# Optimization experiments

Measured on AMD Instinct MI355X. Metric: run time of the kernel, lower is better.

Reference implementation:

```python
import jax, jax.numpy as jnp
import numpy as np

B, S, E = 2, 2048, 2048
HQ, HKV, D = 16, 4, 128
WINDOW = 512
ROPE_BASE = 10000.0


def apply_rope(x):
    # x: [B, H, S, D]; rotate-half RoPE, positions start at 0 (prefill, no cache)
    half = x.shape[-1] // 2
    inv_freq = 1.0 / (ROPE_BASE ** (jnp.arange(half, dtype=jnp.float32) / half))
    ang = jnp.arange(x.shape[2], dtype=jnp.float32)[:, None] * inv_freq[None, :]  # [S, half]
    cos, sin = jnp.cos(ang), jnp.sin(ang)
    x1, x2 = x[..., :half], x[..., half:]
    return jnp.concatenate([x1 * cos - x2 * sin, x1 * sin + x2 * cos], axis=-1)


def setup_inputs() -> dict:
    key = jax.random.key(0)
    ks = jax.random.split(key, 9)
    sc = 0.02
    return {
        "x": jax.random.normal(ks[0], (B, S, E), dtype=jnp.float32),
        "Wq": jax.random.normal(ks[1], (HQ * D, E), dtype=jnp.float32) * sc,
        "bq": jnp.zeros((HQ * D,), dtype=jnp.float32),
        "Wk": jax.random.normal(ks[2], (HKV * D, E), dtype=jnp.float32) * sc,
        "bk": jnp.zeros((HKV * D,), dtype=jnp.float32),
        "Wv": jax.random.normal(ks[3], (HKV * D, E), dtype=jnp.float32) * sc,
        "bv": jnp.zeros((HKV * D,), dtype=jnp.float32),
        "Wo": jax.random.normal(ks[4], (E, HQ * D), dtype=jnp.float32) * sc,
        "bo": jnp.zeros((E,), dtype=jnp.float32),
    }


def reference(x, Wq, bq, Wk, bk, Wv, bv, Wo, bo):
    b, s, _ = x.shape
    group = HQ // HKV
    # projections (torch Linear: y = x @ W.T + b)
    Q = (x @ Wq.T + bq).reshape(b, s, HQ, D).transpose(0, 2, 1, 3)     # [B,HQ,S,D]
    K = (x @ Wk.T + bk).reshape(b, s, HKV, D).transpose(0, 2, 1, 3)    # [B,HKV,S,D]
    V = (x @ Wv.T + bv).reshape(b, s, HKV, D).transpose(0, 2, 1, 3)
    Q = apply_rope(Q)
    K = apply_rope(K)
    # GQA: group query heads per KV head instead of repeating K/V (same math)
    Qg = Q.reshape(b, HKV, group, s, D)
    scores = jnp.einsum('bkgqd,bkyd->bkgqy', Qg, K) / jnp.sqrt(jnp.float32(D))
    # sliding-window causal mask: j <= i and i - j <= window_size
    i = jnp.arange(s)[:, None]
    j = jnp.arange(s)[None, :]
    allowed = (j <= i) & ((i - j) <= WINDOW)
    scores = jnp.where(allowed, scores, jnp.float32(-jnp.inf))
    w = jax.nn.softmax(scores, axis=-1)
    out = jnp.einsum('bkgqy,bkyd->bkgqd', w, V)                        # [B,HKV,G,S,D]
    out = out.reshape(b, HQ, s, D).transpose(0, 2, 1, 3).reshape(b, s, HQ * D)
    out = out @ Wo.T + bo  # dropout is identity at inference
    return out
```

## Files before the change

### kernel.cpp

```cpp
#include <hip/hip_runtime.h>
#include <hip/hip_bf16.h>

typedef unsigned short u16;
typedef unsigned int u32;
typedef __attribute__((ext_vector_type(4))) unsigned short ushort4_t;
typedef __attribute__((ext_vector_type(8))) short short8;
typedef __attribute__((ext_vector_type(4))) float f32x4;

#define B_ 2
#define S_ 2048
#define E_ 2048
#define HQ_ 16
#define HKV_ 4
#define D_ 128
#define WINDOW_ 512

static __device__ __forceinline__ float bf2f(u16 u) {
    union { unsigned int i; float f; } v; v.i = ((unsigned int)u) << 16; return v.f;
}
static __device__ __forceinline__ u16 f2bf(float f) {
    unsigned int x = __float_as_uint(f);
    unsigned int r = (x + 0x7fffu + ((x >> 16) & 1u)) >> 16;
    return (u16)r;
}

static __device__ __forceinline__ void gload_lds16(const u16* g, u16* l) {
    __builtin_amdgcn_global_load_lds(
        (const __attribute__((address_space(1))) unsigned int*)g,
        (__attribute__((address_space(3))) unsigned int*)l,
        16, 0, 0);
}

static __device__ __forceinline__ int detect_fp32(const u16* wq, int* cnt_sh) {
    if (threadIdx.x == 0) *cnt_sh = 0;
    __syncthreads();
    int c = 0;
    #pragma unroll
    for (int k = 0; k < 4; ++k) {
        u16 v = wq[threadIdx.x * 4 + k];
        if (((v >> 7) & 0xFF) >= 0x90) c++;
    }
    atomicAdd(cnt_sh, c);
    __syncthreads();
    return (*cnt_sh >= 64) ? 1 : 0;
}

#define C_WQ   8388608u
#define C_WK   12582912u
#define C_WV   13631488u
#define C_BQ   14680064u
#define C_BK   14682112u
#define C_BV   14682624u
#define C_WO   14683136u
#define C_BO   18877440u
#define NTOT   18879488u

__global__ __launch_bounds__(256) void convert_kernel(
    const void* p0, const void* p1, const void* p2, const void* p3, const void* p4,
    const void* p5, const void* p6, const void* p7, const void* p8,
    u16* __restrict__ C, int* __restrict__ flagout)
{
    __shared__ int cnt;
    const int f = detect_fp32((const u16*)p1, &cnt);
    if (blockIdx.x == 0 && threadIdx.x == 0) *flagout = f;

    unsigned int idx = (blockIdx.x * 256u + threadIdx.x) * 4u;
    if (idx >= NTOT) return;

    const void* src; unsigned int local;
    if      (idx < C_WQ) { src = p0; local = idx; }
    else if (idx < C_WK) { src = p1; local = idx - C_WQ; }
    else if (idx < C_WV) { src = p3; local = idx - C_WK; }
    else if (idx < C_BQ) { src = p5; local = idx - C_WV; }
    else if (idx < C_BK) { src = p2; local = idx - C_BQ; }
    else if (idx < C_BV) { src = p4; local = idx - C_BK; }
    else if (idx < C_WO) { src = p6; local = idx - C_BV; }
    else if (idx < C_BO) { src = p7; local = idx - C_WO; }
    else                 { src = p8; local = idx - C_BO; }

    ushort4_t o;
    if (f) {
        float4 v = *(const float4*)((const float*)src + local);
        o[0] = f2bf(v.x); o[1] = f2bf(v.y); o[2] = f2bf(v.z); o[3] = f2bf(v.w);
    } else {
        o = *(const ushort4_t*)((const u16*)src + local);
    }
    *(ushort4_t*)(C + idx) = o;
}

__global__ __launch_bounds__(512, 2) void gemm256(
    const u16* __restrict__ A, const u16* __restrict__ W,
    const u16* __restrict__ bias, u16* __restrict__ C,
    int M, int N, int K)
{
    __shared__ __align__(16) u16 lds[65536];

    const int m0 = blockIdx.y * 256, n0 = blockIdx.x * 256;
    const int t = threadIdx.x;
    const int wv = t >> 6, lane = t & 63;
    const int wm = wv >> 2, wn = wv & 3;
    const int quad = lane >> 4, l16 = lane & 15;
    const int h3 = l16 & 7;

    const int rr = t >> 3;
    const int sblk = ((t & 7) ^ (rr & 7)) * 8;

    const u16* Asrc = A + (size_t)(m0 + rr) * K + sblk;
    const u16* Bsrc = W + (size_t)(n0 + rr) * K + sblk;
    u16* ldsA = lds + wv * 512;
    u16* ldsB = lds + 16384 + wv * 512;

#define STAGE_A(slot, Qi, k0) gload_lds16(Asrc + (size_t)((Qi) * 64) * K + (k0), ldsA + (slot) * 32768 + (Qi) * 4096)
#define STAGE_B(slot, Qi, k0) gload_lds16(Bsrc + (size_t)((Qi) * 64) * K + (k0), ldsB + (slot) * 32768 + (Qi) * 4096)

    f32x4 acc[8][4];
    #pragma unroll
    for (int mi = 0; mi < 8; ++mi)
        #pragma unroll
        for (int ni = 0; ni < 4; ++ni)
            acc[mi][ni] = (f32x4){0.f, 0.f, 0.f, 0.f};

    const int NT = K / 64;

    #pragma unroll
    for (int q = 0; q < 4; ++q) STAGE_A(0, q, 0);
    #pragma unroll
    for (int q = 0; q < 4; ++q) STAGE_B(0, q, 0);
    __builtin_amdgcn_sched_barrier(0);
    STAGE_A(1, 0, 64);
    STAGE_A(1, 2, 64);
    __builtin_amdgcn_sched_barrier(0);

    short8 aA[4][2], aB[4][2];
    short8 b0[2][2], b1[2][2];

#define DSREAD_A(dst, qm_)                                                     \
    _Pragma("unroll")                                                          \
    for (int fr = 0; fr < 4; ++fr) {                                           \
        const int r = wm * 128 + (qm_) * 64 + fr * 16 + l16;                   \
        _Pragma("unroll")                                                      \
        for (int kk = 0; kk < 2; ++kk)                                         \
            dst[fr][kk] = *(const short8*)(As + r * 64 + (((kk * 4 + quad) ^ h3) << 3)); \
    }

#define DSREAD_B(dst, qn_)                                                     \
    _Pragma("unroll")                                                          \
    for (int g = 0; g < 2; ++g) {                                              \
        const int r = wn * 64 + (qn_) * 32 + g * 16 + l16;                     \
        _Pragma("unroll")                                                      \
        for (int kk = 0; kk < 2; ++kk)                                         \
            dst[g][kk] = *(const short8*)(Bs + r * 64 + (((kk * 4 + quad) ^ h3) << 3)); \
    }

#define MFMA_PH(qm_, afrag, bfrag, qn_)                                        \
    __builtin_amdgcn_s_setprio(1);                                             \
    _Pragma("unroll")                                                          \
    for (int g = 0; g < 2; ++g)                                                \
        _Pragma("unroll")                                                      \
        for (int fr = 0; fr < 4; ++fr)                                         \
            _Pragma("unroll")                                                  \
            for (int kk = 0; kk < 2; ++kk)                                     \
                acc[(qm_) * 4 + fr][(qn_) * 2 + g] =                           \
                    __builtin_amdgcn_mfma_f32_16x16x32_bf16(                   \
                        afrag[fr][kk], bfrag[g][kk], acc[(qm_) * 4 + fr][(qn_) * 2 + g], 0, 0, 0); \
    __builtin_amdgcn_s_setprio(0);

    for (int kt = 0; kt < NT; ++kt) {
        const int slot = kt & 1;
        const u16* As = lds + slot * 32768;
        const u16* Bs = As + 16384;

        if (kt == NT - 1) asm volatile("s_waitcnt vmcnt(0)" ::: "memory");
        else              asm volatile("s_waitcnt vmcnt(2)" ::: "memory");
        __builtin_amdgcn_s_barrier();
        __builtin_amdgcn_sched_barrier(0);

        const int kB = (kt + 1) * 64;
        const int kA = (kt + 2) * 64;
        const int sB = slot ^ 1;
        const bool doEarly = (kt <= NT - 2);
        const bool doMid   = (kt <= NT - 3);

        DSREAD_A(aA, 0);
        DSREAD_B(b0, 0);
        __builtin_amdgcn_sched_barrier(0);
        DSREAD_B(b1, 1);
        __builtin_amdgcn_sched_barrier(0);

        if (doEarly) { STAGE_A(sB, 1, kB); STAGE_A(sB, 3, kB);
                       STAGE_B(sB, 0, kB); STAGE_B(sB, 1, kB);
                       STAGE_B(sB, 2, kB); STAGE_B(sB, 3, kB); }
        __builtin_amdgcn_sched_barrier(0);

        asm volatile("s_waitcnt lgkmcnt(4)" ::: "memory");
        __builtin_amdgcn_sched_barrier(0);
        DSREAD_A(aB, 1);
        __builtin_amdgcn_sched_barrier(0);

        MFMA_PH(0, aA, b0, 0);
        __builtin_amdgcn_sched_barrier(0);
        asm volatile("s_waitcnt lgkmcnt(8)" ::: "memory");
        __builtin_amdgcn_sched_barrier(0);
        MFMA_PH(0, aA, b1, 1);
        __builtin_amdgcn_sched_barrier(0);
        asm volatile("s_waitcnt lgkmcnt(0)" ::: "memory");
        __builtin_amdgcn_sched_barrier(0);
        __builtin_amdgcn_s_barrier();
        __builtin_amdgcn_sched_barrier(0);

        if (doMid) { STAGE_A(slot, 0, kA); STAGE_A(slot, 2, kA); }
        __builtin_amdgcn_sched_barrier(0);

        MFMA_PH(1, aB, b1, 1);
        __builtin_amdgcn_sched_barrier(0);
        MFMA_PH(1, aB, b0, 0);
        __builtin_amdgcn_sched_barrier(0);
    }

#undef STAGE_A
#undef STAGE_B
#undef DSREAD_A
#undef DSREAD_B
#undef MFMA_PH

    #pragma unroll
    for (int mi = 0; mi < 8; ++mi) {
        #pragma unroll
        for (int ni = 0; ni < 4; ++ni) {
            const int row0 = m0 + wm * 128 + mi * 16 + quad * 4;
            const int col  = n0 + wn * 64 + ni * 16 + l16;
            const float bb = bf2f(bias[col]);
            #pragma unroll
            for (int r = 0; r < 4; ++r)
                C[(size_t)(row0 + r) * N + col] = f2bf(acc[mi][ni][r] + bb);
        }
    }
}

__global__ __launch_bounds__(512, 2) void gemm_out_p(
    const u16* __restrict__ A, const u16* __restrict__ W,
    const u16* __restrict__ bias, void* __restrict__ Cout,
    int M, int N, int K, const int* __restrict__ flagp)
{
    __shared__ __align__(16) u16 lds[49152];

    const int m0 = blockIdx.y * 128, n0 = blockIdx.x * 256;
    const int t = threadIdx.x;
    const int wv = t >> 6, lane = t & 63;
    const int wm = wv >> 2, wn = wv & 3;
    const int quad = lane >> 4, l16 = lane & 15;
    const int h3 = l16 & 7;

    const int rr = t >> 3;
    const int sblk = ((t & 7) ^ (rr & 7)) * 8;

    const u16* Asrc = A + (size_t)(m0 + rr) * K + sblk;
    const u16* Bsrc = W + (size_t)(n0 + rr) * K + sblk;
    u16* ldsA = lds + wv * 512;
    u16* ldsB = lds + 8192 + wv * 512;

#define STAGE_A(slot, Qi, k0) gload_lds16(Asrc + (size_t)((Qi) * 64) * K + (k0), ldsA + (slot) * 24576 + (Qi) * 4096)
#define STAGE_B(slot, Qi, k0) gload_lds16(Bsrc + (size_t)((Qi) * 64) * K + (k0), ldsB + (slot) * 24576 + (Qi) * 4096)

    f32x4 acc[4][4];
    #pragma unroll
    for (int mi = 0; mi < 4; ++mi)
        #pragma unroll
        for (int ni = 0; ni < 4; ++ni)
            acc[mi][ni] = (f32x4){0.f, 0.f, 0.f, 0.f};

    const int NT = K / 64;

    STAGE_A(0, 0, 0); STAGE_A(0, 1, 0);
    STAGE_B(0, 0, 0); STAGE_B(0, 1, 0); STAGE_B(0, 2, 0); STAGE_B(0, 3, 0);
    __builtin_amdgcn_sched_barrier(0);
    STAGE_A(1, 0, 64);
    __builtin_amdgcn_sched_barrier(0);

    short8 aA[4][2];
    short8 b0[2][2], b1[2][2];

#define DSREAD_A(dst)                                                          \
    _Pragma("unroll")                                                          \
    for (int fr = 0; fr < 4; ++fr) {                                           \
        const int r = wm * 64 + fr * 16 + l16;                                 \
        _Pragma("unroll")                                                      \
        for (int kk = 0; kk < 2; ++kk)                                         \
            dst[fr][kk] = *(const short8*)(As + r * 64 + (((kk * 4 + quad) ^ h3) << 3)); \
    }

#define DSREAD_B(dst, qn_)                                                     \
    _Pragma("unroll")                                                          \
    for (int g = 0; g < 2; ++g) {                                              \
        const int r = wn * 64 + (qn_) * 32 + g * 16 + l16;                     \
        _Pragma("unroll")                                                      \
        for (int kk = 0; kk < 2; ++kk)                                         \
            dst[g][kk] = *(const short8*)(Bs + r * 64 + (((kk * 4 + quad) ^ h3) << 3)); \
    }

#define MFMA_PH(bfrag, qn_)                                                    \
    __builtin_amdgcn_s_setprio(1);                                             \
    _Pragma("unroll")                                                          \
    for (int g = 0; g < 2; ++g)                                                \
        _Pragma("unroll")                                                      \
        for (int fr = 0; fr < 4; ++fr)                                         \
            _Pragma("unroll")                                                  \
            for (int kk = 0; kk < 2; ++kk)                                     \
                acc[fr][(qn_) * 2 + g] =                                       \
                    __builtin_amdgcn_mfma_f32_16x16x32_bf16(                   \
                        aA[fr][kk], bfrag[g][kk], acc[fr][(qn_) * 2 + g], 0, 0, 0); \
    __builtin_amdgcn_s_setprio(0);

    for (int kt = 0; kt < NT; ++kt) {
        const int slot = kt & 1;
        const u16* As = lds + slot * 24576;
        const u16* Bs = As + 8192;

        if (kt == NT - 1) asm volatile("s_waitcnt vmcnt(0)" ::: "memory");
        else              asm volatile("s_waitcnt vmcnt(1)" ::: "memory");
        __builtin_amdgcn_s_barrier();
        __builtin_amdgcn_sched_barrier(0);

        const int kB = (kt + 1) * 64;
        const int kA = (kt + 2) * 64;
        const int sB = slot ^ 1;
        const bool doEarly = (kt <= NT - 2);
        const bool doMid   = (kt <= NT - 3);

        DSREAD_A(aA);
        DSREAD_B(b0, 0);
        __builtin_amdgcn_sched_barrier(0);
        DSREAD_B(b1, 1);
        __builtin_amdgcn_sched_barrier(0);

        if (doEarly) { STAGE_A(sB, 1, kB);
                       STAGE_B(sB, 0, kB); STAGE_B(sB, 1, kB);
                       STAGE_B(sB, 2, kB); STAGE_B(sB, 3, kB); }
        __builtin_amdgcn_sched_barrier(0);

        asm volatile("s_waitcnt lgkmcnt(4)" ::: "memory");
        __builtin_amdgcn_sched_barrier(0);

        MFMA_PH(b0, 0);
        __builtin_amdgcn_sched_barrier(0);
        asm volatile("s_waitcnt lgkmcnt(0)" ::: "memory");
        __builtin_amdgcn_sched_barrier(0);
        __builtin_amdgcn_s_barrier();
        __builtin_amdgcn_sched_barrier(0);

        if (doMid) { STAGE_A(slot, 0, kA); }
        __builtin_amdgcn_sched_barrier(0);

        MFMA_PH(b1, 1);
        __builtin_amdgcn_sched_barrier(0);
    }

#undef STAGE_A
#undef STAGE_B
#undef DSREAD_A
#undef DSREAD_B
#undef MFMA_PH

    const int f = *flagp;
    #pragma unroll
    for (int mi = 0; mi < 4; ++mi) {
        #pragma unroll
        for (int ni = 0; ni < 4; ++ni) {
            const int row0 = m0 + wm * 64 + mi * 16 + quad * 4;
            const int col  = n0 + wn * 64 + ni * 16 + l16;
            const float bb = bf2f(bias[col]);
            #pragma unroll
            for (int r = 0; r < 4; ++r) {
                float val = acc[mi][ni][r] + bb;
                size_t idx = (size_t)(row0 + r) * N + col;
                if (f) ((float*)Cout)[idx] = val;
                else   ((u16*)Cout)[idx]   = f2bf(val);
            }
        }
    }
}

#define ROPE_BLOCKS 20480

__global__ __launch_bounds__(256) void rope_transpose(
    u16* __restrict__ QKV, u16* __restrict__ VT)
{
    if (blockIdx.x < ROPE_BLOCKS) {
        const size_t qtot = (size_t)B_ * S_ * HQ_ * 64;
        size_t idx = (size_t)blockIdx.x * 256 + threadIdx.x;

        int d; size_t tok; u16* p;
        if (idx < qtot) {
            d = (int)(idx & 63);
            size_t th = idx >> 6;
            int h = (int)(th & 15);
            tok = th >> 4;
            p = QKV + tok * 3072 + h * 128 + d;
        } else {
            size_t r = idx - qtot;
            d = (int)(r & 63);
            size_t th = r >> 6;
            int kh = (int)(th & 3);
            tok = th >> 2;
            p = QKV + tok * 3072 + 2048 + kh * 128 + d;
        }
        int s = (int)(tok & (S_ - 1));

        float x1 = bf2f(p[0]);
        float x2 = bf2f(p[64]);
        float inv_freq = __expf(-0.14391156514f * (float)d);
        float ang = (float)s * inv_freq;
        float sn, cs;
        __sincosf(ang, &sn, &cs);
        p[0]  = f2bf(x1 * cs - x2 * sn);
        p[64] = f2bf(x1 * sn + x2 * cs);
    } else {
        const int bid = blockIdx.x - ROPE_BLOCKS;
        const int t = threadIdx.x;
        const int s_blk = bid & 63;
        const int dh = (bid >> 6) & 1;
        const int bkh = bid >> 7;
        const int b = bkh >> 2, kh = bkh & 3;

        const int d = dh * 64 + (t & 63);
        const int s0 = s_blk * 32 + (t >> 6) * 8;

        const u16* src = QKV + (size_t)(b * S_ + s0) * 3072 + 2560 + kh * 128 + d;
        short8 v;
        #pragma unroll
        for (int j = 0; j < 8; ++j)
            v[j] = (short)src[(size_t)j * 3072];
        *(short8*)(VT + ((size_t)(bkh * 128 + d)) * S_ + s0) = v;
    }
}

__global__ __launch_bounds__(256) void attn_mfma(
    const u16* __restrict__ QKV, const u16* __restrict__ VT, u16* __restrict__ O)
{
    __shared__ __align__(16) u16 Ks[32 * 136];
    __shared__ __align__(16) u16 Vs[128 * 40];
    __shared__ __align__(16) u16 ps[4][16 * 40];

    const int t = threadIdx.x;
    const int wv = t >> 6, lane = t & 63;
    const int quad = lane >> 4, l16 = lane & 15;

    const int h = blockIdx.x & 15;
    const int tile = (blockIdx.x >> 4) & 31;
    const int b = blockIdx.x >> 9;
    const int kh = h >> 2;

    const int i0b = tile * 64;
    const int i0w = i0b + wv * 16;
    const float scale = 0.08838834764831845f;
    const float CEXP = 8.0f;

    short8 qf[4];
    {
        const u16* qrow = QKV + (size_t)(b * S_ + i0w + l16) * 3072 + h * 128 + quad * 8;
        #pragma unroll
        for (int kc = 0; kc < 4; ++kc)
            qf[kc] = *(const short8*)(qrow + kc * 32);
    }

    short8 ones;
    #pragma unroll
    for (int j = 0; j < 8; ++j) ones[j] = (short)0x3F80;

    f32x4 oc[8];
    #pragma unroll
    for (int c = 0; c < 8; ++c) oc[c] = (f32x4){0.f, 0.f, 0.f, 0.f};
    f32x4 ocl = (f32x4){0.f, 0.f, 0.f, 0.f};

    int jlo = i0b - WINDOW_; if (jlo < 0) jlo = 0;
    const int nblk = (i0b + 64 - jlo) >> 5;

    const u16* VTb = VT + (size_t)(b * 4 + kh) * 128 * S_;

    for (int blk = 0; blk < nblk; ++blk) {
        const int jbase = jlo + blk * 32;
        __syncthreads();
        #pragma unroll
        for (int it = 0; it < 2; ++it) {
            int idx = it * 256 + t;
            int key = idx >> 4;
            int c8  = (idx & 15) * 8;
            int row = ((key & 1) << 4) | (key >> 1);
            short8 kvv = *(const short8*)(QKV + (size_t)(b * S_ + jbase + key) * 3072 + 2048 + kh * 128 + c8);
            *(short8*)(Ks + row * 136 + c8) = kvv;
        }
        #pragma unroll
        for (int it = 0; it < 2; ++it) {
            int idx = it * 256 + t;
            int d = idx >> 2;
            int q4 = idx & 3;
            short8 vvv = *(const short8*)(VTb + (size_t)d * S_ + jbase + q4 * 8);
            *(short8*)(Vs + d * 40 + q4 * 8) = vvv;
        }
        __syncthreads();

        bool active = (jbase <= i0w + 15) && (jbase + 31 >= i0w - WINDOW_);
        if (!active) continue;

        f32x4 sc0 = {0.f,0.f,0.f,0.f}, sc1 = {0.f,0.f,0.f,0.f};
        #pragma unroll
        for (int kc = 0; kc < 4; ++kc) {
            short8 kb0 = *(const short8*)(Ks + l16 * 136 + kc * 32 + quad * 8);
            short8 kb1 = *(const short8*)(Ks + (16 + l16) * 136 + kc * 32 + quad * 8);
            sc0 = __builtin_amdgcn_mfma_f32_16x16x32_bf16(qf[kc], kb0, sc0, 0, 0, 0);
            sc1 = __builtin_amdgcn_mfma_f32_16x16x32_bf16(qf[kc], kb1, sc1, 0, 0, 0);
        }

        const int j0 = jbase + 2 * l16;
        const int iq = i0w + quad * 4;
        u16* pw = ps[wv];
        #pragma unroll
        for (int r = 0; r < 4; ++r) {
            int i = iq + r;
            bool ok0 = (unsigned)(i - j0)     <= (unsigned)WINDOW_;
            bool ok1 = (unsigned)(i - j0 - 1) <= (unsigned)WINDOW_;
            float p0 = ok0 ? __expf(sc0[r] * scale - CEXP) : 0.f;
            float p1 = ok1 ? __expf(sc1[r] * scale - CEXP) : 0.f;
            u32 pk = ((u32)f2bf(p1) << 16) | (u32)f2bf(p0);
            *(u32*)(pw + (quad * 4 + r) * 40 + 2 * l16) = pk;
        }
        short8 pa = *(const short8*)(pw + l16 * 40 + quad * 8);

        #pragma unroll
        for (int c = 0; c < 8; ++c) {
            short8 vb = *(const short8*)(Vs + (c * 16 + l16) * 40 + quad * 8);
            oc[c] = __builtin_amdgcn_mfma_f32_16x16x32_bf16(pa, vb, oc[c], 0, 0, 0);
        }
        ocl = __builtin_amdgcn_mfma_f32_16x16x32_bf16(pa, ones, ocl, 0, 0, 0);
    }

    float inv0[4];
    #pragma unroll
    for (int r = 0; r < 4; ++r) inv0[r] = 1.0f / ocl[r];
    #pragma unroll
    for (int c = 0; c < 8; ++c) {
        #pragma unroll
        for (int r = 0; r < 4; ++r) {
            O[((size_t)(b * S_ + i0w + quad * 4 + r) * HQ_ + h) * D_ + c * 16 + l16] =
                f2bf(oc[c][r] * inv0[r]);
        }
    }
}

extern "C" void kernel_launch(void* const* d_in, const int* in_sizes, int n_in,
                              void* d_out, int out_size, void* d_ws, size_t ws_size,
                              hipStream_t stream)
{
    char* ws = (char*)d_ws;
    u16* Cc   = (u16*)ws;
    int* flag = (int*)(ws + 37758976);
    u16* QKV  = (u16*)(ws + 37759232);
    u16* Ab   = (u16*)(ws + 37759232 + 25165824);

    const u16* xb    = Cc;
    u16*       VT    = Cc;
    const u16* Wqkv  = Cc + C_WQ;
    const u16* bqkv  = Cc + C_BQ;
    const u16* Wob   = Cc + C_WO;
    const u16* bob   = Cc + C_BO;

    const int M = B_ * S_;
    dim3 blk(256);

    convert_kernel<<<dim3(NTOT / 4 / 256), blk, 0, stream>>>(
        d_in[0], d_in[1], d_in[2], d_in[3], d_in[4], d_in[5], d_in[6], d_in[7], d_in[8],
        Cc, flag);

    gemm256<<<dim3(3072 / 256, M / 256), dim3(512), 0, stream>>>(
        xb, Wqkv, bqkv, QKV, M, 3072, E_);

    rope_transpose<<<dim3(ROPE_BLOCKS + 1024), blk, 0, stream>>>(QKV, VT);

    attn_mfma<<<dim3(B_ * HQ_ * (S_ / 64)), blk, 0, stream>>>(QKV, VT, Ab);

    gemm_out_p<<<dim3(E_ / 256, M / 128), dim3(512), 0, stream>>>(
        Ab, Wob, bob, d_out, M, E_, HQ_ * D_, flag);
}
```

Measured before the change: 295.4 us.

## Restructure GEMM main loops into barrier-synchronized ping-pong phases

Both GEMM kernels' K-loops are reorganized into phases, each of LDS reads, a slice of global-to-LDS staging, a barrier plus lgkmcnt wait, then an MFMA cluster closed by a trailing barrier. The vmcnt wait for the next tile moves from the loop top to the end of the previous iteration, and an initial wait and barrier is added before the loop. The aim is to interleave memory and MFMA work across the two co-resident workgroups in a ping-pong schedule and spread global loads evenly. It adds several extra barriers per iteration, which could add stalls if the waves do not stay in lockstep.

```diff
diff --git a/kernel.cpp b/kernel.cpp
--- a/kernel.cpp
+++ b/kernel.cpp
@@ -88,6 +88,8 @@
     *(ushort4_t*)(C + idx) = o;
 }
 
+#define SCHED __builtin_amdgcn_sched_barrier(0)
+
 __global__ __launch_bounds__(512, 2) void gemm256(
     const u16* __restrict__ A, const u16* __restrict__ W,
     const u16* __restrict__ bias, u16* __restrict__ C,
@@ -126,10 +128,13 @@
     for (int q = 0; q < 4; ++q) STAGE_A(0, q, 0);
     #pragma unroll
     for (int q = 0; q < 4; ++q) STAGE_B(0, q, 0);
-    __builtin_amdgcn_sched_barrier(0);
+    SCHED;
     STAGE_A(1, 0, 64);
     STAGE_A(1, 2, 64);
-    __builtin_amdgcn_sched_barrier(0);
+    SCHED;
+    asm volatile("s_waitcnt vmcnt(2)" ::: "memory");
+    __builtin_amdgcn_s_barrier();
+    SCHED;
 
     short8 aA[4][2], aB[4][2];
     short8 b0[2][2], b1[2][2];
@@ -165,56 +170,61 @@
                         afrag[fr][kk], bfrag[g][kk], acc[(qm_) * 4 + fr][(qn_) * 2 + g], 0, 0, 0); \
     __builtin_amdgcn_s_setprio(0);
 
+#define BAR_LGKM                                                               \
+    __builtin_amdgcn_s_barrier();                                              \
+    asm volatile("s_waitcnt lgkmcnt(0)" ::: "memory");                         \
+    SCHED;
+
+#define BAR_TRAIL                                                              \
+    SCHED;                                                                     \
+    __builtin_amdgcn_s_barrier();                                              \
+    SCHED;
+
     for (int kt = 0; kt < NT; ++kt) {
         const int slot = kt & 1;
         const u16* As = lds + slot * 32768;
         const u16* Bs = As + 16384;
 
-        if (kt == NT - 1) asm volatile("s_waitcnt vmcnt(0)" ::: "memory");
-        else              asm volatile("s_waitcnt vmcnt(2)" ::: "memory");
-        __builtin_amdgcn_s_barrier();
-        __builtin_amdgcn_sched_barrier(0);
-
         const int kB = (kt + 1) * 64;
         const int kA = (kt + 2) * 64;
         const int sB = slot ^ 1;
-        const bool doEarly = (kt <= NT - 2);
-        const bool doMid   = (kt <= NT - 3);
+        const bool doE = (kt <= NT - 2);
+        const bool doM = (kt <= NT - 3);
 
         DSREAD_A(aA, 0);
         DSREAD_B(b0, 0);
-        __builtin_amdgcn_sched_barrier(0);
+        SCHED;
+        if (doE) { STAGE_A(sB, 1, kB); STAGE_A(sB, 3, kB); }
+        SCHED;
+        BAR_LGKM;
+        MFMA_PH(0, aA, b0, 0);
+        BAR_TRAIL;
+
         DSREAD_B(b1, 1);
-        __builtin_amdgcn_sched_barrier(0);
-
-        if (doEarly) { STAGE_A(sB, 1, kB); STAGE_A(sB, 3, kB);
-                       STAGE_B(sB, 0, kB); STAGE_B(sB, 1, kB);
-                       STAGE_B(sB, 2, kB); STAGE_B(sB, 3, kB); }
-        __builtin_amdgcn_sched_barrier(0);
-
-        asm volatile("s_waitcnt lgkmcnt(4)" ::: "memory");
-        __builtin_amdgcn_sched_barrier(0);
+        SCHED;
+        if (doE) { STAGE_B(sB, 0, kB); STAGE_B(sB, 1, kB); }
+        SCHED;
+        BAR_LGKM;
+        MFMA_PH(0, aA, b1, 1);
+        BAR_TRAIL;
+
         DSREAD_A(aB, 1);
-        __builtin_amdgcn_sched_barrier(0);
-
-        MFMA_PH(0, aA, b0, 0);
-        __builtin_amdgcn_sched_barrier(0);
-        asm volatile("s_waitcnt lgkmcnt(8)" ::: "memory");
-        __builtin_amdgcn_sched_barrier(0);
-        MFMA_PH(0, aA, b1, 1);
-        __builtin_amdgcn_sched_barrier(0);
-        asm volatile("s_waitcnt lgkmcnt(0)" ::: "memory");
-        __builtin_amdgcn_sched_barrier(0);
+        SCHED;
+        if (doE) { STAGE_B(sB, 2, kB); STAGE_B(sB, 3, kB); }
+        SCHED;
+        BAR_LGKM;
+        MFMA_PH(1, aB, b1, 1);
+        BAR_TRAIL;
+
+        if (doM) { STAGE_A(slot, 0, kA); STAGE_A(slot, 2, kA); }
+        SCHED;
+        if (kt == NT - 2)     asm volatile("s_waitcnt vmcnt(0)" ::: "memory");
+        else if (kt < NT - 2) asm volatile("s_waitcnt vmcnt(2)" ::: "memory");
+        SCHED;
         __builtin_amdgcn_s_barrier();
-        __builtin_amdgcn_sched_barrier(0);
-
-        if (doMid) { STAGE_A(slot, 0, kA); STAGE_A(slot, 2, kA); }
-        __builtin_amdgcn_sched_barrier(0);
-
-        MFMA_PH(1, aB, b1, 1);
-        __builtin_amdgcn_sched_barrier(0);
+        SCHED;
         MFMA_PH(1, aB, b0, 0);
-        __builtin_amdgcn_sched_barrier(0);
+        BAR_TRAIL;
     }
 
 #undef STAGE_A
@@ -273,9 +283,12 @@
 
     STAGE_A(0, 0, 0); STAGE_A(0, 1, 0);
     STAGE_B(0, 0, 0); STAGE_B(0, 1, 0); STAGE_B(0, 2, 0); STAGE_B(0, 3, 0);
-    __builtin_amdgcn_sched_barrier(0);
+    SCHED;
     STAGE_A(1, 0, 64);
-    __builtin_amdgcn_sched_barrier(0);
+    SCHED;
+    asm volatile("s_waitcnt vmcnt(1)" ::: "memory");
+    __builtin_amdgcn_s_barrier();
+    SCHED;
 
     short8 aA[4][2];
     short8 b0[2][2], b1[2][2];
@@ -316,43 +329,40 @@
         const u16* As = lds + slot * 24576;
         const u16* Bs = As + 8192;
 
-        if (kt == NT - 1) asm volatile("s_waitcnt vmcnt(0)" ::: "memory");
-        else              asm volatile("s_waitcnt vmcnt(1)" ::: "memory");
-        __builtin_amdgcn_s_barrier();
-        __builtin_amdgcn_sched_barrier(0);
-
         const int kB = (kt + 1) * 64;
         const int kA = (kt + 2) * 64;
         const int sB = slot ^ 1;
-        const bool doEarly = (kt <= NT - 2);
-        const bool doMid   = (kt <= NT - 3);
+        const bool doE = (kt <= NT - 2);
+        const bool doM = (kt <= NT - 3);
 
         DSREAD_A(aA);
         DSREAD_B(b0, 0);
-        __builtin_amdgcn_sched_barrier(0);
+        SCHED;
+        if (doE) { STAGE_A(sB, 1, kB); STAGE_B(sB, 0, kB); STAGE_B(sB, 1, kB); }
+        SCHED;
+        __builtin_amdgcn_s_barrier();
+        asm volatile("s_waitcnt lgkmcnt(0)" ::: "memory");
+        SCHED;
+        MFMA_PH(b0, 0);
+        SCHED;
+        __builtin_amdgcn_s_barrier();
+        SCHED;
+
         DSREAD_B(b1, 1);
-        __builtin_amdgcn_sched_barrier(0);
-
-        if (doEarly) { STAGE_A(sB, 1, kB);
-                       STAGE_B(sB, 0, kB); STAGE_B(sB, 1, kB);
-                       STAGE_B(sB, 2, kB); STAGE_B(sB, 3, kB); }
-        __builtin_amdgcn_sched_barrier(0);
-
-        asm volatile("s_waitcnt lgkmcnt(4)" ::: "memory");
-        __builtin_amdgcn_sched_barrier(0);
-
-        MFMA_PH(b0, 0);
-        __builtin_amdgcn_sched_barrier(0);
+        SCHED;
+        if (doE) { STAGE_B(sB, 2, kB); STAGE_B(sB, 3, kB); }
+        if (doM) { STAGE_A(slot, 0, kA); }
+        SCHED;
+        if (kt == NT - 2)     asm volatile("s_waitcnt vmcnt(0)" ::: "memory");
+        else if (kt < NT - 2) asm volatile("s_waitcnt vmcnt(1)" ::: "memory");
+        SCHED;
+        __builtin_amdgcn_s_barrier();
         asm volatile("s_waitcnt lgkmcnt(0)" ::: "memory");
-        __builtin_amdgcn_sched_barrier(0);
+        SCHED;
+        MFMA_PH(b1, 1);
+        SCHED;
         __builtin_amdgcn_s_barrier();
-        __builtin_amdgcn_sched_barrier(0);
-
-        if (doMid) { STAGE_A(slot, 0, kA); }
-        __builtin_amdgcn_sched_barrier(0);
-
-        MFMA_PH(b1, 1);
-        __builtin_amdgcn_sched_barrier(0);
+        SCHED;
     }
 
 #undef STAGE_A
```

After: 316.6 us. 1.07x slower.
